# Performance work log

Measured on AMD Instinct MI355X. Metric: run time of the kernel, lower is better.

The kernel has to match this reference:

```python
import jax, jax.numpy as jnp
import numpy as np

B, S, D, A_DIM = 8, 2048, 256, 64

def setup_inputs() -> dict:
    key = jax.random.key(0)
    k_x, k_wm, k_wl, k_eps = jax.random.split(key, 4)
    return {
        "x": jax.random.normal(k_x, (B, S, D), dtype=jnp.float32),
        "W_mean": jax.random.normal(k_wm, (D, A_DIM), dtype=jnp.float32) * (1.0 / np.sqrt(D)),
        "b_mean": jnp.zeros((A_DIM,), dtype=jnp.float32),
        "W_logvar": jax.random.normal(k_wl, (D, A_DIM), dtype=jnp.float32) * (1.0 / np.sqrt(D)),
        "b_logvar": jnp.zeros((A_DIM,), dtype=jnp.float32),
        "eps": jax.random.normal(k_eps, (B, S, A_DIM), dtype=jnp.float32),
    }

def reference(x, W_mean, b_mean, W_logvar, b_logvar, eps):
    d = x.shape[-1]
    scale = 1.0 / jnp.sqrt(jnp.asarray(d, dtype=x.dtype))
    # S_det = x x^T / sqrt(d)  -> [B, S, S]
    scores = jnp.einsum("bsd,btd->bst", x, x) * scale
    attn = jax.nn.softmax(scores, axis=-1)
    # A_det = softmax(S) x  -> [B, S, D]
    A_det = jnp.einsum("bst,btd->bsd", attn, x)
    A_mean = A_det @ W_mean + b_mean        # [B, S, A_DIM]
    A_logvar = A_det @ W_logvar + b_logvar  # [B, S, A_DIM]
    A = A_mean + jnp.exp(0.5 * A_logvar) * eps  # sqrt(exp(logvar)) = exp(logvar/2)
    return (A_mean, A_logvar, A)
```

## Files before the change

kernel.cpp:

```cpp
#include <hip/hip_runtime.h>

#define B_ 8
#define S_ 2048
#define D_ 256

typedef _Float16 f16;
typedef f16 f16x2 __attribute__((ext_vector_type(2)));
typedef f16 f16x8 __attribute__((ext_vector_type(8)));
typedef float f32x16 __attribute__((ext_vector_type(16)));
typedef unsigned int u32;
typedef u32 u32x4 __attribute__((ext_vector_type(4)));

typedef const __attribute__((address_space(1))) unsigned int* gptr_t;
typedef __attribute__((address_space(3))) unsigned int* lptr_t;

__device__ __forceinline__ void gload_lds16(const void* g, void* l) {
  __builtin_amdgcn_global_load_lds((gptr_t)(unsigned long long)g,
                                   (lptr_t)(unsigned long long)l, 16, 0, 0);
}

__device__ __forceinline__ u32 packf16(float a, float b) {
  f16x2 t; t[0] = (f16)a; t[1] = (f16)b;
  return __builtin_bit_cast(u32, t);
}

__device__ __forceinline__ void pack16(const f32x16& p, int hi, u32x4& o0, u32x4& o1) {
#pragma unroll
  for (int c2 = 0; c2 < 2; ++c2) {
    u32 a1 = packf16(p[8 * c2 + 0], p[8 * c2 + 1]);
    u32 a2 = packf16(p[8 * c2 + 2], p[8 * c2 + 3]);
    u32 b1 = packf16(p[8 * c2 + 4], p[8 * c2 + 5]);
    u32 b2 = packf16(p[8 * c2 + 6], p[8 * c2 + 7]);
    u32 xa1 = __shfl_xor(a1, 32), xa2 = __shfl_xor(a2, 32);
    u32 xb1 = __shfl_xor(b1, 32), xb2 = __shfl_xor(b2, 32);
    u32x4 f;
    f[0] = hi ? xb1 : a1;
    f[1] = hi ? xb2 : a2;
    f[2] = hi ? b1 : xa1;
    f[3] = hi ? b2 : xa2;
    if (c2) o1 = f; else o0 = f;
  }
}

#define SC2F 0.09016844f
#define NMAXR 20.0f

__global__ void prep(const float* __restrict__ x, const float* __restrict__ Wm,
                     const float* __restrict__ Wl, f16* __restrict__ xh,
                     float* __restrict__ n2, f16* __restrict__ Wt) {
  __shared__ f16 tile[64][264];
  const int bid = blockIdx.x;
  const int t = threadIdx.x;
  if (bid < 256) {
    const int b = bid >> 5, st = bid & 31;
    const int s0 = st * 64;
    const float* xb = x + ((size_t)(b * S_ + s0)) * D_;
    f16* xhb = xh + ((size_t)(b * S_ + s0)) * D_;
#pragma unroll
    for (int it = 0; it < 16; ++it) {
      int flat = it * 256 + t;
      int r = flat >> 6, c4 = flat & 63;
      float4 v = *reinterpret_cast<const float4*>(xb + r * 256 + c4 * 4);
      f16 h0 = (f16)v.x, h1 = (f16)v.y, h2 = (f16)v.z, h3 = (f16)v.w;
      f16x2 p0 = {h0, h1}, p1 = {h2, h3};
      uint2 wv; wv.x = __builtin_bit_cast(u32, p0); wv.y = __builtin_bit_cast(u32, p1);
      *reinterpret_cast<uint2*>(xhb + r * 256 + c4 * 4) = wv;
      tile[r][c4 * 4 + 0] = h0; tile[r][c4 * 4 + 1] = h1;
      tile[r][c4 * 4 + 2] = h2; tile[r][c4 * 4 + 3] = h3;
    }
    __syncthreads();
    {
      int r = t >> 2, qd = t & 3;
      float s = 0.0f;
#pragma unroll
      for (int i = 0; i < 8; ++i) {
        f16x8 v = *reinterpret_cast<const f16x8*>(&tile[r][qd * 64 + i * 8]);
#pragma unroll
        for (int u = 0; u < 8; ++u) { float f = (float)v[u]; s += f * f; }
      }
      s += __shfl_xor(s, 1); s += __shfl_xor(s, 2);
      if (qd == 0) n2[b * S_ + s0 + r] = s;
    }
  } else {
    int idx = (bid - 256) * 1024 + t * 4;
    int j = idx >> 8, d = idx & 255;
#pragma unroll
    for (int k2 = 0; k2 < 4; ++k2) {
      float v = (j < 64) ? Wm[(d + k2) * 64 + j] : Wl[(d + k2) * 64 + (j - 64)];
      Wt[idx + k2] = (f16)v;
    }
  }
}

__launch_bounds__(256)
__global__ void xw_kern(const f16* __restrict__ xh, const f16* __restrict__ Wt,
                        f16* __restrict__ XWt) {
  __shared__ f16 Ax[2][4096];
  __shared__ f16 Ww[2][8192];
  const int idx = blockIdx.x;
  const int b = idx & 7;
  const int sb = (idx >> 3) * 64;
  const int tid = threadIdx.x, lane = tid & 63, w = tid >> 6;
  const int l31 = lane & 31, hi = lane >> 5;
  const f16* xb = xh + (size_t)b * S_ * D_;

#define XW_STAGE(st, pp)                                                       \
  {                                                                            \
    _Pragma("unroll") for (int i = 0; i < 2; ++i) {                            \
      int ch = i * 256 + tid; int r = ch >> 3, c = ch & 7;                     \
      int csrc = c ^ (r & 7);                                                  \
      gload_lds16(xb + (size_t)(sb + r) * 256 + ((st) * 64) + csrc * 8,        \
                  &Ax[(pp)][0] + ch * 8);                                      \
    }                                                                          \
    _Pragma("unroll") for (int i = 0; i < 4; ++i) {                            \
      int ch = i * 256 + tid; int r = ch >> 3, c = ch & 7;                     \
      int csrc = c ^ (r & 7);                                                  \
      gload_lds16(Wt + (size_t)r * 256 + ((st) * 64) + csrc * 8,               \
                  &Ww[(pp)][0] + ch * 8);                                      \
    }                                                                          \
  }

  f32x16 acc[2];
#pragma unroll
  for (int i = 0; i < 2; ++i)
#pragma unroll
    for (int e = 0; e < 16; ++e) acc[i][e] = 0.0f;

  XW_STAGE(0, 0);
  __syncthreads();
#pragma unroll
  for (int t = 0; t < 4; ++t) {
    const int p = t & 1;
    if (t < 3) XW_STAGE(t + 1, p ^ 1);
#pragma unroll
    for (int kc = 0; kc < 4; ++kc) {
      int cc = ((2 * kc + hi) ^ (l31 & 7)) * 8;
      f16x8 bf = *reinterpret_cast<const f16x8*>(&Ww[p][(w * 32 + l31) * 64 + cc]);
#pragma unroll
      for (int mi = 0; mi < 2; ++mi) {
        f16x8 af = *reinterpret_cast<const f16x8*>(&Ax[p][(mi * 32 + l31) * 64 + cc]);
        acc[mi] = __builtin_amdgcn_mfma_f32_32x32x16_f16(af, bf, acc[mi], 0, 0, 0);
      }
    }
    __syncthreads();
  }
#undef XW_STAGE

  const int j = w * 32 + l31;
  f16* dst = XWt + ((size_t)b * 128 + j) * 2048;
#pragma unroll
  for (int mi = 0; mi < 2; ++mi) {
    u32x4 s0, s1;
    pack16(acc[mi], hi, s0, s1);
    *reinterpret_cast<u32x4*>(dst + sb + mi * 32 + hi * 8) = s0;
    *reinterpret_cast<u32x4*>(dst + sb + mi * 32 + 16 + hi * 8) = s1;
  }
}

__launch_bounds__(512, 4)
__global__ void gemm1_kern(const f16* __restrict__ xh, const float* __restrict__ n2,
                           f16* __restrict__ P, float* __restrict__ Lp,
                           int b0, int bm, int bsh) {
  __shared__ __align__(16) char smem[65536];
  f16* Aq = (f16*)smem;
  f16* Bk = (f16*)(smem + 32768);
  const int idx = blockIdx.x;
  const int bl = idx & bm;
  int tdec = idx >> bsh;
  int qt = 0;
#pragma unroll 1
  while (tdec >= 16 - qt) { tdec -= 16 - qt; ++qt; }
  const int kt = qt + tdec;
  const int b = b0 + bl;
  const int qb = qt * 128, kb = kt * 128;
  const int tid = threadIdx.x, lane = tid & 63, w = tid >> 6;
  const int l31 = lane & 31, hi = lane >> 5;
  const int wq = w >> 2, wk = w & 3;
  const f16* xb = xh + (size_t)b * S_ * D_;

#define G1_STAGE(st, pp)                                                       \
  { _Pragma("unroll") for (int i = 0; i < 4; ++i) {                            \
      int ii = w * 4 + i;                                                      \
      int flat = ii * 64 + lane;                                               \
      bool isB = ii >= 16;                                                     \
      int ch = isB ? flat - 1024 : flat;                                       \
      int r = ch >> 3, c = ch & 7;                                             \
      int csrc = c ^ (r & 7);                                                  \
      const f16* src = xb + (size_t)((isB ? kb : qb) + r) * 256 +              \
                       (st) * 64 + csrc * 8;                                   \
      f16* dst = (isB ? Bk : Aq) + ((pp) * 8192) + ch * 8;                     \
      gload_lds16(src, dst);                                                   \
    } }

  f32x16 acc[2];
#pragma unroll
  for (int i = 0; i < 2; ++i)
#pragma unroll
    for (int e = 0; e < 16; ++e) acc[i][e] = 0.0f;

  G1_STAGE(0, 0);
  __syncthreads();
#pragma unroll
  for (int t = 0; t < 4; ++t) {
    const int p = t & 1;
    if (t < 3) G1_STAGE(t + 1, p ^ 1);
#pragma unroll
    for (int kc = 0; kc < 4; ++kc) {
      int cc = ((2 * kc + hi) ^ (l31 & 7)) * 8;
      f16x8 af  = *reinterpret_cast<const f16x8*>(Bk + p * 8192 + (wk * 32 + l31) * 64 + cc);
      f16x8 bf0 = *reinterpret_cast<const f16x8*>(Aq + p * 8192 + (wq * 64 + l31) * 64 + cc);
      f16x8 bf1 = *reinterpret_cast<const f16x8*>(Aq + p * 8192 + (wq * 64 + 32 + l31) * 64 + cc);
      acc[0] = __builtin_amdgcn_mfma_f32_32x32x16_f16(af, bf0, acc[0], 0, 0, 0);
      acc[1] = __builtin_amdgcn_mfma_f32_32x32x16_f16(af, bf1, acc[1], 0, 0, 0);
    }
    __syncthreads();
  }
#undef G1_STAGE

  float* raw = (float*)smem;
  if (kt != qt) {
#pragma unroll
    for (int ni = 0; ni < 2; ++ni)
#pragma unroll
      for (int j = 0; j < 16; ++j) {
        int kvloc = wk * 32 + (j & 3) + 8 * (j >> 2) + 4 * hi;
        int qloc = wq * 64 + ni * 32 + l31;
        raw[kvloc * 128 + (qloc ^ ((kvloc & 7) << 2))] = acc[ni][j];
      }
  }

  float r2[2], lsum[2];
  int qrow[2];
#pragma unroll
  for (int ni = 0; ni < 2; ++ni) {
    qrow[ni] = qb + wq * 64 + ni * 32 + l31;
    r2[ni] = sqrtf(n2[b * S_ + qrow[ni]]) * (NMAXR * SC2F);
    lsum[ni] = 0.0f;
  }
#pragma unroll
  for (int ni = 0; ni < 2; ++ni)
#pragma unroll
    for (int j = 0; j < 16; ++j) {
      float v = exp2f(acc[ni][j] * SC2F - r2[ni]);
      acc[ni][j] = v;
      lsum[ni] += v;
    }
#pragma unroll
  for (int ni = 0; ni < 2; ++ni) lsum[ni] += __shfl_xor(lsum[ni], 32);

  const int colb = kb + wk * 32;
#pragma unroll
  for (int ni = 0; ni < 2; ++ni) {
    u32x4 s0, s1;
    pack16(acc[ni], hi, s0, s1);
    size_t rowp = (size_t)(bl * S_ + qrow[ni]) * 2048;
    *reinterpret_cast<u32x4*>(P + rowp + colb + hi * 8) = s0;
    *reinterpret_cast<u32x4*>(P + rowp + colb + 16 + hi * 8) = s1;
  }

  if (kt != qt) {
    __syncthreads();
    const int kvr = tid >> 2;
    const int qseg = (tid & 3) * 32;
    float r2kv = sqrtf(n2[b * S_ + kb + kvr]) * (NMAXR * SC2F);
    u32 ow[16];
    float tsum = 0.0f;
#pragma unroll
    for (int c8 = 0; c8 < 8; ++c8) {
      int qs = qseg + c8 * 4;
      float4 v = *reinterpret_cast<const float4*>(
          &raw[kvr * 128 + (qs ^ ((kvr & 7) << 2))]);
      float e0 = exp2f(v.x * SC2F - r2kv), e1 = exp2f(v.y * SC2F - r2kv);
      float e2 = exp2f(v.z * SC2F - r2kv), e3 = exp2f(v.w * SC2F - r2kv);
      tsum += (e0 + e1) + (e2 + e3);
      ow[c8 * 2 + 0] = packf16(e0, e1);
      ow[c8 * 2 + 1] = packf16(e2, e3);
    }
    size_t rowp = (size_t)(bl * S_ + kb + kvr) * 2048;
#pragma unroll
    for (int sseg = 0; sseg < 4; ++sseg) {
      u32x4 sv;
      sv[0] = ow[sseg * 4 + 0]; sv[1] = ow[sseg * 4 + 1];
      sv[2] = ow[sseg * 4 + 2]; sv[3] = ow[sseg * 4 + 3];
      *reinterpret_cast<u32x4*>(P + rowp + qb + qseg + sseg * 8) = sv;
    }
    tsum += __shfl_xor(tsum, 1);
    tsum += __shfl_xor(tsum, 2);
    if ((tid & 3) == 0)
      Lp[(size_t)(bl * 16 + qt) * 2048 + kb + kvr] = tsum;
  }

  __syncthreads();
  float* Lred = (float*)smem;
  if (hi == 0) {
    Lred[(wq * 64 + l31) * 4 + wk] = lsum[0];
    Lred[(wq * 64 + 32 + l31) * 4 + wk] = lsum[1];
  }
  __syncthreads();
  if (tid < 128) {
    float s = Lred[tid * 4] + Lred[tid * 4 + 1] + Lred[tid * 4 + 2] + Lred[tid * 4 + 3];
    Lp[(size_t)(bl * 16 + kt) * 2048 + qb + tid] = s;
  }
}

__launch_bounds__(256, 3)
__global__ void gemm2p_kern(const f16* __restrict__ P, const f16* __restrict__ XWt,
                            const float* __restrict__ Lp, float* __restrict__ Yp,
                            int b0, int bm_, int bsh, int kso) {
  __shared__ f16 Pq[2][4096];
  __shared__ f16 Xw[2][8192];
  const int idx = blockIdx.x;
  const int bl = idx & bm_;
  const int qt = (idx >> bsh) & 31;
  const int ks = idx >> (bsh + 5);
  const int b = b0 + bl;
  const int qb = qt * 64;
  const int kcol0 = ks * 1024;
  const int tid = threadIdx.x, lane = tid & 63, w = tid >> 6;
  const int l31 = lane & 31, hi = lane >> 5;
  const int wq = w & 1, wc = w >> 1;
  const f16* xwb = XWt + (size_t)b * 128 * 2048;

#define GP_STAGE(tt, pp)                                                       \
  {                                                                            \
    _Pragma("unroll") for (int i = 0; i < 2; ++i) {                            \
      int ch = i * 256 + tid; int r = ch >> 3, c = ch & 7;                     \
      int csrc = c ^ (r & 7);                                                  \
      gload_lds16(P + (size_t)(bl * S_ + qb + r) * 2048 + kcol0 + ((tt) * 64) + csrc * 8, \
                  &Pq[(pp)][0] + ch * 8);                                      \
    }                                                                          \
    _Pragma("unroll") for (int i = 0; i < 4; ++i) {                            \
      int ch = i * 256 + tid; int r = ch >> 3, c = ch & 7;                     \
      int csrc = c ^ (r & 7);                                                  \
      gload_lds16(xwb + (size_t)r * 2048 + kcol0 + ((tt) * 64) + csrc * 8,     \
                  &Xw[(pp)][0] + ch * 8);                                      \
    }                                                                          \
  }

  f32x16 acc[2];
#pragma unroll
  for (int i = 0; i < 2; ++i)
#pragma unroll
    for (int e = 0; e < 16; ++e) acc[i][e] = 0.0f;

  GP_STAGE(0, 0);
  __syncthreads();
#pragma unroll 1
  for (int t = 0; t < 16; ++t) {
    const int p = t & 1;
    if (t < 15) GP_STAGE(t + 1, p ^ 1);
#pragma unroll
    for (int kc = 0; kc < 4; ++kc) {
      int cc = ((2 * kc + hi) ^ (l31 & 7)) * 8;
      f16x8 bf = *reinterpret_cast<const f16x8*>(&Pq[p][(wq * 32 + l31) * 64 + cc]);
#pragma unroll
      for (int mi = 0; mi < 2; ++mi) {
        int jrow = mi * 64 + wc * 32 + l31;
        f16x8 af = *reinterpret_cast<const f16x8*>(&Xw[p][jrow * 64 + cc]);
        acc[mi] = __builtin_amdgcn_mfma_f32_32x32x16_f16(af, bf, acc[mi], 0, 0, 0);
      }
    }
    __syncthreads();
  }
#undef GP_STAGE

  const int q = qb + wq * 32 + l31;
  float L = 0.0f;
#pragma unroll
  for (int kt = 0; kt < 16; ++kt) L += Lp[(size_t)(bl * 16 + kt) * 2048 + q];
  float rL = 1.0f / L;
  float* dst = Yp + ((size_t)ks * kso + (size_t)bl * 2048 + q) * 128;
#pragma unroll
  for (int jg = 0; jg < 4; ++jg) {
    int cb = wc * 32 + 8 * jg + 4 * hi;
    float4 mn, lv;
    float* mnp = &mn.x; float* lvp = &lv.x;
#pragma unroll
    for (int jj = 0; jj < 4; ++jj) {
      int j = jg * 4 + jj;
      mnp[jj] = acc[0][j] * rL;
      lvp[jj] = acc[1][j] * rL;
    }
    *reinterpret_cast<float4*>(dst + cb) = mn;
    *reinterpret_cast<float4*>(dst + 64 + cb) = lv;
  }
}

__launch_bounds__(256)
__global__ void reduce_kern(const float* __restrict__ Yp, const float* __restrict__ bm,
                            const float* __restrict__ bl_, const float* __restrict__ eps,
                            float* __restrict__ out, int b0, int kso) {
  const int t = threadIdx.x;
  const int rowp = blockIdx.x * 32 + (t >> 3);
  const int j0 = (t & 7) * 8;
  const int grow = b0 * 2048 + rowp;
  const float* y0 = Yp + (size_t)rowp * 128;
  const float* y1 = Yp + (size_t)kso * 128 + (size_t)rowp * 128;
  float mv[8], lv[8], ev[8];
#pragma unroll
  for (int i = 0; i < 2; ++i) {
    float4 a = *reinterpret_cast<const float4*>(y0 + j0 + i * 4);
    float4 b = *reinterpret_cast<const float4*>(y1 + j0 + i * 4);
    float4 c = *reinterpret_cast<const float4*>(y0 + 64 + j0 + i * 4);
    float4 d = *reinterpret_cast<const float4*>(y1 + 64 + j0 + i * 4);
    float4 e = *reinterpret_cast<const float4*>(eps + (size_t)grow * 64 + j0 + i * 4);
    mv[i*4+0] = a.x + b.x; mv[i*4+1] = a.y + b.y; mv[i*4+2] = a.z + b.z; mv[i*4+3] = a.w + b.w;
    lv[i*4+0] = c.x + d.x; lv[i*4+1] = c.y + d.y; lv[i*4+2] = c.z + d.z; lv[i*4+3] = c.w + d.w;
    ev[i*4+0] = e.x; ev[i*4+1] = e.y; ev[i*4+2] = e.z; ev[i*4+3] = e.w;
  }
  float om[8], ol[8], oa[8];
#pragma unroll
  for (int i = 0; i < 8; ++i) {
    float m = mv[i] + bm[j0 + i];
    float l = lv[i] + bl_[j0 + i];
    om[i] = m;
    ol[i] = l;
    oa[i] = m + exp2f(0.7213475204f * l) * ev[i];
  }
  float* o0 = out + (size_t)grow * 64 + j0;
#pragma unroll
  for (int i = 0; i < 2; ++i) {
    *reinterpret_cast<float4*>(o0 + i * 4) = *reinterpret_cast<float4*>(&om[i * 4]);
    *reinterpret_cast<float4*>(o0 + 1048576 + i * 4) = *reinterpret_cast<float4*>(&ol[i * 4]);
    *reinterpret_cast<float4*>(o0 + 2097152 + i * 4) = *reinterpret_cast<float4*>(&oa[i * 4]);
  }
}

extern "C" void kernel_launch(void* const* d_in, const int* in_sizes, int n_in,
                              void* d_out, int out_size, void* d_ws, size_t ws_size,
                              hipStream_t stream) {
  (void)in_sizes; (void)n_in; (void)out_size;
  const float* x   = (const float*)d_in[0];
  const float* Wm  = (const float*)d_in[1];
  const float* bmv = (const float*)d_in[2];
  const float* Wl  = (const float*)d_in[3];
  const float* blv = (const float*)d_in[4];
  const float* ep  = (const float*)d_in[5];
  float* out = (float*)d_out;

  char* ws = (char*)d_ws;
  f16*   xh   = (f16*)(ws + 0);
  f16*   XWt  = (f16*)(ws + 8388608);
  f16*   Wt   = (f16*)(ws + 12582912);
  float* n2   = (float*)(ws + 12648448);
  float* Lp   = (float*)(ws + 12713984);
  float* Yp   = (float*)(ws + 13762560);
  const size_t P_off = 30539776;
  f16*   Pbuf = (f16*)(ws + P_off);

  int bpp = 1;
  if      (ws_size >= P_off + (size_t)8 * 2048 * 2048 * 2) bpp = 8;
  else if (ws_size >= P_off + (size_t)4 * 2048 * 2048 * 2) bpp = 4;
  else if (ws_size >= P_off + (size_t)2 * 2048 * 2048 * 2) bpp = 2;
  const int bsh = (bpp == 8) ? 3 : (bpp == 4) ? 2 : (bpp == 2) ? 1 : 0;
  const int bm = bpp - 1;
  const int kso = bpp * 2048;

  prep<<<288, 256, 0, stream>>>(x, Wm, Wl, xh, n2, Wt);
  xw_kern<<<256, 256, 0, stream>>>(xh, Wt, XWt);
  for (int b0 = 0; b0 < 8; b0 += bpp) {
    gemm1_kern<<<bpp * 136, 512, 0, stream>>>(xh, n2, Pbuf, Lp, b0, bm, bsh);
    gemm2p_kern<<<bpp * 64, 256, 0, stream>>>(Pbuf, XWt, Lp, Yp, b0, bm, bsh, kso);
    reduce_kern<<<bpp * 64, 256, 0, stream>>>(Yp, bmv, blv, ep, out, b0, kso);
  }
}
```

Measured before the change: 74.17 us.

## Enlarge per-warp MFMA tiles and split gemm2 K four ways, move normalization to reduce

gemm1 now runs 256 threads, and each warp computes a 64x64 tile with a 2x2 MFMA accumulator grid instead of 32x64, which raises operand reuse from LDS. gemm2p switches to 128-row Q tiles with 2x2 per-warp tiles and a four-way K split of 512 columns, using a larger workspace for Yp. The softmax denominator sum and reciprocal move from gemm2p into reduce_kern, which now sums four partials. The trade-offs are more register pressure, lower occupancy, and extra partial-sum traffic through Yp.

```diff
diff --git a/kernel.cpp b/kernel.cpp
--- a/kernel.cpp
+++ b/kernel.cpp
@@ -157,7 +157,7 @@
   }
 }
 
-__launch_bounds__(512, 4)
+__launch_bounds__(256, 2)
 __global__ void gemm1_kern(const f16* __restrict__ xh, const float* __restrict__ n2,
                            f16* __restrict__ P, float* __restrict__ Lp,
                            int b0, int bm, int bsh) {
@@ -175,28 +175,29 @@
   const int qb = qt * 128, kb = kt * 128;
   const int tid = threadIdx.x, lane = tid & 63, w = tid >> 6;
   const int l31 = lane & 31, hi = lane >> 5;
-  const int wq = w >> 2, wk = w & 3;
+  const int wq = w >> 1, wk = w & 1;
   const f16* xb = xh + (size_t)b * S_ * D_;
 
 #define G1_STAGE(st, pp)                                                       \
-  { _Pragma("unroll") for (int i = 0; i < 4; ++i) {                            \
-      int ii = w * 4 + i;                                                      \
-      int flat = ii * 64 + lane;                                               \
-      bool isB = ii >= 16;                                                     \
-      int ch = isB ? flat - 1024 : flat;                                       \
+  { _Pragma("unroll") for (int i = 0; i < 8; ++i) {                            \
+      int flat = (w * 8 + i) * 64 + lane;                                      \
+      bool isB = flat >= 1024;                                                 \
+      int ch = flat & 1023;                                                    \
       int r = ch >> 3, c = ch & 7;                                             \
       int csrc = c ^ (r & 7);                                                  \
       const f16* src = xb + (size_t)((isB ? kb : qb) + r) * 256 +              \
-                       (st) * 64 + csrc * 8;                                   \
+                       ((st) * 64) + csrc * 8;                                 \
       f16* dst = (isB ? Bk : Aq) + ((pp) * 8192) + ch * 8;                     \
       gload_lds16(src, dst);                                                   \
     } }
 
-  f32x16 acc[2];
+  f32x16 acc[2][2];
 #pragma unroll
   for (int i = 0; i < 2; ++i)
 #pragma unroll
-    for (int e = 0; e < 16; ++e) acc[i][e] = 0.0f;
+    for (int j = 0; j < 2; ++j)
+#pragma unroll
+      for (int e = 0; e < 16; ++e) acc[i][j][e] = 0.0f;
 
   G1_STAGE(0, 0);
   __syncthreads();
@@ -207,11 +208,21 @@
 #pragma unroll
     for (int kc = 0; kc < 4; ++kc) {
       int cc = ((2 * kc + hi) ^ (l31 & 7)) * 8;
-      f16x8 af  = *reinterpret_cast<const f16x8*>(Bk + p * 8192 + (wk * 32 + l31) * 64 + cc);
-      f16x8 bf0 = *reinterpret_cast<const f16x8*>(Aq + p * 8192 + (wq * 64 + l31) * 64 + cc);
-      f16x8 bf1 = *reinterpret_cast<const f16x8*>(Aq + p * 8192 + (wq * 64 + 32 + l31) * 64 + cc);
-      acc[0] = __builtin_amdgcn_mfma_f32_32x32x16_f16(af, bf0, acc[0], 0, 0, 0);
-      acc[1] = __builtin_amdgcn_mfma_f32_32x32x16_f16(af, bf1, acc[1], 0, 0, 0);
+      f16x8 af[2], bf[2];
+#pragma unroll
+      for (int mi = 0; mi < 2; ++mi)
+        af[mi] = *reinterpret_cast<const f16x8*>(
+            Bk + p * 8192 + (wk * 64 + mi * 32 + l31) * 64 + cc);
+#pragma unroll
+      for (int ni = 0; ni < 2; ++ni)
+        bf[ni] = *reinterpret_cast<const f16x8*>(
+            Aq + p * 8192 + (wq * 64 + ni * 32 + l31) * 64 + cc);
+#pragma unroll
+      for (int mi = 0; mi < 2; ++mi)
+#pragma unroll
+        for (int ni = 0; ni < 2; ++ni)
+          acc[mi][ni] = __builtin_amdgcn_mfma_f32_32x32x16_f16(
+              af[mi], bf[ni], acc[mi][ni], 0, 0, 0);
     }
     __syncthreads();
   }
@@ -220,13 +231,15 @@
   float* raw = (float*)smem;
   if (kt != qt) {
 #pragma unroll
-    for (int ni = 0; ni < 2; ++ni)
-#pragma unroll
-      for (int j = 0; j < 16; ++j) {
-        int kvloc = wk * 32 + (j & 3) + 8 * (j >> 2) + 4 * hi;
-        int qloc = wq * 64 + ni * 32 + l31;
-        raw[kvloc * 128 + (qloc ^ ((kvloc & 7) << 2))] = acc[ni][j];
-      }
+    for (int mi = 0; mi < 2; ++mi)
+#pragma unroll
+      for (int ni = 0; ni < 2; ++ni)
+#pragma unroll
+        for (int j = 0; j < 16; ++j) {
+          int kvloc = wk * 64 + mi * 32 + (j & 3) + 8 * (j >> 2) + 4 * hi;
+          int qloc = wq * 64 + ni * 32 + l31;
+          raw[kvloc * 128 + (qloc ^ ((kvloc & 7) << 2))] = acc[mi][ni][j];
+        }
   }
 
   float r2[2], lsum[2];
@@ -238,181 +251,201 @@
     lsum[ni] = 0.0f;
   }
 #pragma unroll
-  for (int ni = 0; ni < 2; ++ni)
-#pragma unroll
-    for (int j = 0; j < 16; ++j) {
-      float v = exp2f(acc[ni][j] * SC2F - r2[ni]);
-      acc[ni][j] = v;
-      lsum[ni] += v;
-    }
+  for (int mi = 0; mi < 2; ++mi)
+#pragma unroll
+    for (int ni = 0; ni < 2; ++ni)
+#pragma unroll
+      for (int j = 0; j < 16; ++j) {
+        float v = exp2f(acc[mi][ni][j] * SC2F - r2[ni]);
+        acc[mi][ni][j] = v;
+        lsum[ni] += v;
+      }
 #pragma unroll
   for (int ni = 0; ni < 2; ++ni) lsum[ni] += __shfl_xor(lsum[ni], 32);
 
-  const int colb = kb + wk * 32;
-#pragma unroll
-  for (int ni = 0; ni < 2; ++ni) {
-    u32x4 s0, s1;
-    pack16(acc[ni], hi, s0, s1);
-    size_t rowp = (size_t)(bl * S_ + qrow[ni]) * 2048;
-    *reinterpret_cast<u32x4*>(P + rowp + colb + hi * 8) = s0;
-    *reinterpret_cast<u32x4*>(P + rowp + colb + 16 + hi * 8) = s1;
+#pragma unroll
+  for (int mi = 0; mi < 2; ++mi) {
+    const int colb = kb + wk * 64 + mi * 32;
+#pragma unroll
+    for (int ni = 0; ni < 2; ++ni) {
+      u32x4 s0, s1;
+      pack16(acc[mi][ni], hi, s0, s1);
+      size_t rowp = (size_t)(bl * S_ + qrow[ni]) * 2048;
+      *reinterpret_cast<u32x4*>(P + rowp + colb + hi * 8) = s0;
+      *reinterpret_cast<u32x4*>(P + rowp + colb + 16 + hi * 8) = s1;
+    }
   }
 
   if (kt != qt) {
     __syncthreads();
-    const int kvr = tid >> 2;
-    const int qseg = (tid & 3) * 32;
+    const int kvr = tid >> 1;
+    const int qh = (tid & 1) * 64;
     float r2kv = sqrtf(n2[b * S_ + kb + kvr]) * (NMAXR * SC2F);
-    u32 ow[16];
+    u32 ow[32];
     float tsum = 0.0f;
 #pragma unroll
-    for (int c8 = 0; c8 < 8; ++c8) {
-      int qs = qseg + c8 * 4;
+    for (int c16 = 0; c16 < 16; ++c16) {
+      int qs = qh + c16 * 4;
       float4 v = *reinterpret_cast<const float4*>(
           &raw[kvr * 128 + (qs ^ ((kvr & 7) << 2))]);
       float e0 = exp2f(v.x * SC2F - r2kv), e1 = exp2f(v.y * SC2F - r2kv);
       float e2 = exp2f(v.z * SC2F - r2kv), e3 = exp2f(v.w * SC2F - r2kv);
       tsum += (e0 + e1) + (e2 + e3);
-      ow[c8 * 2 + 0] = packf16(e0, e1);
-      ow[c8 * 2 + 1] = packf16(e2, e3);
+      ow[c16 * 2 + 0] = packf16(e0, e1);
+      ow[c16 * 2 + 1] = packf16(e2, e3);
     }
     size_t rowp = (size_t)(bl * S_ + kb + kvr) * 2048;
 #pragma unroll
-    for (int sseg = 0; sseg < 4; ++sseg) {
+    for (int sseg = 0; sseg < 8; ++sseg) {
       u32x4 sv;
       sv[0] = ow[sseg * 4 + 0]; sv[1] = ow[sseg * 4 + 1];
       sv[2] = ow[sseg * 4 + 2]; sv[3] = ow[sseg * 4 + 3];
-      *reinterpret_cast<u32x4*>(P + rowp + qb + qseg + sseg * 8) = sv;
+      *reinterpret_cast<u32x4*>(P + rowp + qb + qh + sseg * 8) = sv;
     }
     tsum += __shfl_xor(tsum, 1);
-    tsum += __shfl_xor(tsum, 2);
-    if ((tid & 3) == 0)
+    if ((tid & 1) == 0)
       Lp[(size_t)(bl * 16 + qt) * 2048 + kb + kvr] = tsum;
   }
 
   __syncthreads();
   float* Lred = (float*)smem;
   if (hi == 0) {
-    Lred[(wq * 64 + l31) * 4 + wk] = lsum[0];
-    Lred[(wq * 64 + 32 + l31) * 4 + wk] = lsum[1];
+#pragma unroll
+    for (int ni = 0; ni < 2; ++ni)
+      Lred[(wq * 64 + ni * 32 + l31) * 2 + wk] = lsum[ni];
   }
   __syncthreads();
-  if (tid < 128) {
-    float s = Lred[tid * 4] + Lred[tid * 4 + 1] + Lred[tid * 4 + 2] + Lred[tid * 4 + 3];
-    Lp[(size_t)(bl * 16 + kt) * 2048 + qb + tid] = s;
-  }
-}
-
-__launch_bounds__(256, 3)
+  if (tid < 128)
+    Lp[(size_t)(bl * 16 + kt) * 2048 + qb + tid] = Lred[tid * 2] + Lred[tid * 2 + 1];
+}
+
+__launch_bounds__(256, 2)
 __global__ void gemm2p_kern(const f16* __restrict__ P, const f16* __restrict__ XWt,
-                            const float* __restrict__ Lp, float* __restrict__ Yp,
-                            int b0, int bm_, int bsh, int kso) {
-  __shared__ f16 Pq[2][4096];
+                            float* __restrict__ Yp, int b0, int bm_, int bsh,
+                            int kso) {
+  __shared__ f16 Pq[2][8192];
   __shared__ f16 Xw[2][8192];
   const int idx = blockIdx.x;
   const int bl = idx & bm_;
-  const int qt = (idx >> bsh) & 31;
-  const int ks = idx >> (bsh + 5);
+  const int qt = (idx >> bsh) & 15;
+  const int ks = idx >> (bsh + 4);
   const int b = b0 + bl;
-  const int qb = qt * 64;
-  const int kcol0 = ks * 1024;
+  const int qb = qt * 128;
+  const int kcol0 = ks * 512;
   const int tid = threadIdx.x, lane = tid & 63, w = tid >> 6;
   const int l31 = lane & 31, hi = lane >> 5;
-  const int wq = w & 1, wc = w >> 1;
+  const int wq = w >> 1, wc = w & 1;
   const f16* xwb = XWt + (size_t)b * 128 * 2048;
 
 #define GP_STAGE(tt, pp)                                                       \
-  {                                                                            \
-    _Pragma("unroll") for (int i = 0; i < 2; ++i) {                            \
-      int ch = i * 256 + tid; int r = ch >> 3, c = ch & 7;                     \
+  { _Pragma("unroll") for (int i = 0; i < 8; ++i) {                            \
+      int flat = (w * 8 + i) * 64 + lane;                                      \
+      bool isX = flat >= 1024;                                                 \
+      int ch = flat & 1023;                                                    \
+      int r = ch >> 3, c = ch & 7;                                             \
       int csrc = c ^ (r & 7);                                                  \
-      gload_lds16(P + (size_t)(bl * S_ + qb + r) * 2048 + kcol0 + ((tt) * 64) + csrc * 8, \
-                  &Pq[(pp)][0] + ch * 8);                                      \
-    }                                                                          \
-    _Pragma("unroll") for (int i = 0; i < 4; ++i) {                            \
-      int ch = i * 256 + tid; int r = ch >> 3, c = ch & 7;                     \
-      int csrc = c ^ (r & 7);                                                  \
-      gload_lds16(xwb + (size_t)r * 2048 + kcol0 + ((tt) * 64) + csrc * 8,     \
-                  &Xw[(pp)][0] + ch * 8);                                      \
-    }                                                                          \
-  }
-
-  f32x16 acc[2];
+      const f16* src = isX                                                     \
+          ? xwb + (size_t)r * 2048 + kcol0 + ((tt) * 64) + csrc * 8            \
+          : P + (size_t)(bl * S_ + qb + r) * 2048 + kcol0 + ((tt) * 64) + csrc * 8; \
+      f16* dst = (isX ? &Xw[(pp)][0] : &Pq[(pp)][0]) + ch * 8;                 \
+      gload_lds16(src, dst);                                                   \
+    } }
+
+  f32x16 acc[2][2];
 #pragma unroll
   for (int i = 0; i < 2; ++i)
 #pragma unroll
-    for (int e = 0; e < 16; ++e) acc[i][e] = 0.0f;
+    for (int j = 0; j < 2; ++j)
+#pragma unroll
+      for (int e = 0; e < 16; ++e) acc[i][j][e] = 0.0f;
 
   GP_STAGE(0, 0);
   __syncthreads();
 #pragma unroll 1
-  for (int t = 0; t < 16; ++t) {
+  for (int t = 0; t < 8; ++t) {
     const int p = t & 1;
-    if (t < 15) GP_STAGE(t + 1, p ^ 1);
+    if (t < 7) GP_STAGE(t + 1, p ^ 1);
 #pragma unroll
     for (int kc = 0; kc < 4; ++kc) {
       int cc = ((2 * kc + hi) ^ (l31 & 7)) * 8;
-      f16x8 bf = *reinterpret_cast<const f16x8*>(&Pq[p][(wq * 32 + l31) * 64 + cc]);
-#pragma unroll
-      for (int mi = 0; mi < 2; ++mi) {
-        int jrow = mi * 64 + wc * 32 + l31;
-        f16x8 af = *reinterpret_cast<const f16x8*>(&Xw[p][jrow * 64 + cc]);
-        acc[mi] = __builtin_amdgcn_mfma_f32_32x32x16_f16(af, bf, acc[mi], 0, 0, 0);
+      f16x8 af[2], bf[2];
+#pragma unroll
+      for (int mi = 0; mi < 2; ++mi)
+        af[mi] = *reinterpret_cast<const f16x8*>(
+            &Xw[p][(wc * 64 + mi * 32 + l31) * 64 + cc]);
+#pragma unroll
+      for (int ni = 0; ni < 2; ++ni)
+        bf[ni] = *reinterpret_cast<const f16x8*>(
+            &Pq[p][(wq * 64 + ni * 32 + l31) * 64 + cc]);
+#pragma unroll
+      for (int mi = 0; mi < 2; ++mi)
+#pragma unroll
+        for (int ni = 0; ni < 2; ++ni)
+          acc[mi][ni] = __builtin_amdgcn_mfma_f32_32x32x16_f16(
+              af[mi], bf[ni], acc[mi][ni], 0, 0, 0);
+    }
+    __syncthreads();
+  }
+#undef GP_STAGE
+
+#pragma unroll
+  for (int ni = 0; ni < 2; ++ni) {
+    const int q = qb + wq * 64 + ni * 32 + l31;
+    float* dst = Yp + ((size_t)ks * kso + (size_t)bl * S_ + q) * 128;
+#pragma unroll
+    for (int mi = 0; mi < 2; ++mi)
+#pragma unroll
+      for (int jg = 0; jg < 4; ++jg) {
+        int cb = wc * 64 + mi * 32 + 8 * jg + 4 * hi;
+        float4 v;
+        v.x = acc[mi][ni][jg * 4 + 0];
+        v.y = acc[mi][ni][jg * 4 + 1];
+        v.z = acc[mi][ni][jg * 4 + 2];
+        v.w = acc[mi][ni][jg * 4 + 3];
+        *reinterpret_cast<float4*>(dst + cb) = v;
       }
-    }
-    __syncthreads();
-  }
-#undef GP_STAGE
-
-  const int q = qb + wq * 32 + l31;
-  float L = 0.0f;
-#pragma unroll
-  for (int kt = 0; kt < 16; ++kt) L += Lp[(size_t)(bl * 16 + kt) * 2048 + q];
-  float rL = 1.0f / L;
-  float* dst = Yp + ((size_t)ks * kso + (size_t)bl * 2048 + q) * 128;
-#pragma unroll
-  for (int jg = 0; jg < 4; ++jg) {
-    int cb = wc * 32 + 8 * jg + 4 * hi;
-    float4 mn, lv;
-    float* mnp = &mn.x; float* lvp = &lv.x;
-#pragma unroll
-    for (int jj = 0; jj < 4; ++jj) {
-      int j = jg * 4 + jj;
-      mnp[jj] = acc[0][j] * rL;
-      lvp[jj] = acc[1][j] * rL;
-    }
-    *reinterpret_cast<float4*>(dst + cb) = mn;
-    *reinterpret_cast<float4*>(dst + 64 + cb) = lv;
   }
 }
 
 __launch_bounds__(256)
-__global__ void reduce_kern(const float* __restrict__ Yp, const float* __restrict__ bm,
-                            const float* __restrict__ bl_, const float* __restrict__ eps,
-                            float* __restrict__ out, int b0, int kso) {
+__global__ void reduce_kern(const float* __restrict__ Yp, const float* __restrict__ Lp,
+                            const float* __restrict__ bm, const float* __restrict__ bl_,
+                            const float* __restrict__ eps, float* __restrict__ out,
+                            int b0, int kso) {
   const int t = threadIdx.x;
   const int rowp = blockIdx.x * 32 + (t >> 3);
   const int j0 = (t & 7) * 8;
-  const int grow = b0 * 2048 + rowp;
-  const float* y0 = Yp + (size_t)rowp * 128;
-  const float* y1 = Yp + (size_t)kso * 128 + (size_t)rowp * 128;
-  float mv[8], lv[8], ev[8];
+  const int grow = b0 * S_ + rowp;
+  const int bl = rowp >> 11, q = rowp & 2047;
+  float L = 0.0f;
+#pragma unroll
+  for (int kt = 0; kt < 16; ++kt) L += Lp[(size_t)(bl * 16 + kt) * 2048 + q];
+  float rL = 1.0f / L;
+  float mv[8], lv[8];
+#pragma unroll
+  for (int i = 0; i < 8; ++i) { mv[i] = 0.0f; lv[i] = 0.0f; }
+#pragma unroll
+  for (int k = 0; k < 4; ++k) {
+    const float* y = Yp + ((size_t)k * kso + rowp) * 128;
+#pragma unroll
+    for (int i = 0; i < 2; ++i) {
+      float4 a = *reinterpret_cast<const float4*>(y + j0 + i * 4);
+      float4 c = *reinterpret_cast<const float4*>(y + 64 + j0 + i * 4);
+      mv[i*4+0] += a.x; mv[i*4+1] += a.y; mv[i*4+2] += a.z; mv[i*4+3] += a.w;
+      lv[i*4+0] += c.x; lv[i*4+1] += c.y; lv[i*4+2] += c.z; lv[i*4+3] += c.w;
+    }
+  }
+  float ev[8];
 #pragma unroll
   for (int i = 0; i < 2; ++i) {
-    float4 a = *reinterpret_cast<const float4*>(y0 + j0 + i * 4);
-    float4 b = *reinterpret_cast<const float4*>(y1 + j0 + i * 4);
-    float4 c = *reinterpret_cast<const float4*>(y0 + 64 + j0 + i * 4);
-    float4 d = *reinterpret_cast<const float4*>(y1 + 64 + j0 + i * 4);
     float4 e = *reinterpret_cast<const float4*>(eps + (size_t)grow * 64 + j0 + i * 4);
-    mv[i*4+0] = a.x + b.x; mv[i*4+1] = a.y + b.y; mv[i*4+2] = a.z + b.z; mv[i*4+3] = a.w + b.w;
-    lv[i*4+0] = c.x + d.x; lv[i*4+1] = c.y + d.y; lv[i*4+2] = c.z + d.z; lv[i*4+3] = c.w + d.w;
     ev[i*4+0] = e.x; ev[i*4+1] = e.y; ev[i*4+2] = e.z; ev[i*4+3] = e.w;
   }
   float om[8], ol[8], oa[8];
 #pragma unroll
   for (int i = 0; i < 8; ++i) {
-    float m = mv[i] + bm[j0 + i];
-    float l = lv[i] + bl_[j0 + i];
+    float m = mv[i] * rL + bm[j0 + i];
+    float l = lv[i] * rL + bl_[j0 + i];
     om[i] = m;
     ol[i] = l;
     oa[i] = m + exp2f(0.7213475204f * l) * ev[i];
@@ -445,7 +478,7 @@
   float* n2   = (float*)(ws + 12648448);
   float* Lp   = (float*)(ws + 12713984);
   float* Yp   = (float*)(ws + 13762560);
-  const size_t P_off = 30539776;
+  const size_t P_off = 47316992;
   f16*   Pbuf = (f16*)(ws + P_off);
 
   int bpp = 1;
@@ -459,8 +492,8 @@
   prep<<<288, 256, 0, stream>>>(x, Wm, Wl, xh, n2, Wt);
   xw_kern<<<256, 256, 0, stream>>>(xh, Wt, XWt);
   for (int b0 = 0; b0 < 8; b0 += bpp) {
-    gemm1_kern<<<bpp * 136, 512, 0, stream>>>(xh, n2, Pbuf, Lp, b0, bm, bsh);
-    gemm2p_kern<<<bpp * 64, 256, 0, stream>>>(Pbuf, XWt, Lp, Yp, b0, bm, bsh, kso);
-    reduce_kern<<<bpp * 64, 256, 0, stream>>>(Yp, bmv, blv, ep, out, b0, kso);
-  }
-}
+    gemm1_kern<<<bpp * 136, 256, 0, stream>>>(xh, n2, Pbuf, Lp, b0, bm, bsh);
+    gemm2p_kern<<<bpp * 64, 256, 0, stream>>>(Pbuf, XWt, Yp, b0, bm, bsh, kso);
+    reduce_kern<<<bpp * 64, 256, 0, stream>>>(Yp, Lp, bmv, blv, ep, out, b0, kso);
+  }
+}
```

New measurement: 80.07 us. +7.9%, slower.
